# Kernel tuning notes

Measured on AMD Instinct MI355X. Metric: run time of the kernel, lower is better.

The kernel has to match this reference:

```python
import jax, jax.numpy as jnp
import numpy as np

N, E, IN_DIM, HID, TOWERS, NG = 20000, 320000, 16, 50, 5, 64
FO = HID // TOWERS  # out channels per tower = 10
EPS_BN = 1e-5
EPS_STD = 1e-5  # PyG StdAggregation: sqrt(relu(var) + 1e-5)


def setup_inputs() -> dict:
    key = jax.random.key(0)
    ks = jax.random.split(key, 24)
    rn = lambda k, shape: jax.random.normal(k, shape, dtype=jnp.float32) * 0.1
    F0, F1 = IN_DIM, HID
    return {
        "x": jax.random.normal(ks[0], (N, IN_DIM), dtype=jnp.float32),
        "edge_index": jax.random.randint(ks[1], (2, E), 0, N),
        "batch": jnp.sort(jax.random.randint(ks[2], (N,), 0, NG)),
        # conv0: pre Linear(2*F0 -> F0) per tower, post Linear(13*F0 -> FO) per tower, lin Linear(HID->HID)
        "pre_W0": rn(ks[3], (TOWERS, F0, 2 * F0)), "pre_b0": rn(ks[4], (TOWERS, F0)),
        "post_W0": rn(ks[5], (TOWERS, FO, 13 * F0)), "post_b0": rn(ks[6], (TOWERS, FO)),
        "lin_W0": rn(ks[7], (HID, HID)), "lin_b0": rn(ks[8], (HID,)),
        "gamma0": jnp.ones((HID,), jnp.float32), "beta0": jnp.zeros((HID,), jnp.float32),
        # conv1
        "pre_W1": rn(ks[9], (TOWERS, F1, 2 * F1)), "pre_b1": rn(ks[10], (TOWERS, F1)),
        "post_W1": rn(ks[11], (TOWERS, FO, 13 * F1)), "post_b1": rn(ks[12], (TOWERS, FO)),
        "lin_W1": rn(ks[13], (HID, HID)), "lin_b1": rn(ks[14], (HID,)),
        "gamma1": jnp.ones((HID,), jnp.float32), "beta1": jnp.zeros((HID,), jnp.float32),
        # head MLP: HID->50->25->1
        "mlp_W1": rn(ks[15], (50, HID)), "mlp_b1": rn(ks[16], (50,)),
        "mlp_W2": rn(ks[17], (25, 50)), "mlp_b2": rn(ks[18], (25,)),
        "mlp_W3": rn(ks[19], (1, 25)), "mlp_b3": rn(ks[20], (1,)),
    }


def pna_conv(x, src, dst, deg, avg_log, pre_W, pre_b, post_W, post_b, lin_W, lin_b):
    # x: [N, F]; divide_input=False -> every tower sees the full F features.
    n, Fi = x.shape
    T = pre_W.shape[0]
    # message: h = cat([x_i, x_j]) = cat([x[dst], x[src]]), then per-tower pre-MLP (1 Linear)
    h = jnp.concatenate([x[dst], x[src]], axis=-1)                  # [E, 2F]
    hs = jnp.einsum('ef,tgf->etg', h, pre_W) + pre_b                # [E, T, F]
    flat = hs.reshape(hs.shape[0], T * Fi)                          # [E, T*F]
    # multi-aggregation: mean / min / max / std, scattered to dst
    s = jax.ops.segment_sum(flat, dst, num_segments=n)
    s2 = jax.ops.segment_sum(flat * flat, dst, num_segments=n)
    mn = jax.ops.segment_min(flat, dst, num_segments=n)
    mx = jax.ops.segment_max(flat, dst, num_segments=n)
    degc = jnp.maximum(deg, 1.0)[:, None]
    mean = s / degc
    var = s2 / degc - mean * mean
    std = jnp.sqrt(jax.nn.relu(var) + EPS_STD)
    has = (deg > 0)[:, None]
    mn = jnp.where(has, mn, 0.0)
    mx = jnp.where(has, mx, 0.0)
    agg = jnp.concatenate([mean.reshape(n, T, Fi), mn.reshape(n, T, Fi),
                           mx.reshape(n, T, Fi), std.reshape(n, T, Fi)], axis=-1)  # [N,T,4F]
    # degree scalers: identity, amplification, attenuation
    amp = (jnp.log(jnp.maximum(deg, 1.0) + 1.0) / avg_log)[:, None, None]
    out = jnp.concatenate([jnp.broadcast_to(x[:, None, :], (n, T, Fi)),
                           agg, agg * amp, agg / amp], axis=-1)      # [N, T, 13F]
    out = jnp.einsum('ntf,tgf->ntg', out, post_W) + post_b          # [N, T, FO]
    return out.reshape(n, T * post_W.shape[1]) @ lin_W.T + lin_b    # [N, HID]


def _bn_relu(h, g, b):
    mu = h.mean(axis=0)
    v = jnp.mean((h - mu) ** 2, axis=0)  # biased var, torch BN training-mode normalization
    return jax.nn.relu(g * (h - mu) / jnp.sqrt(v + EPS_BN) + b)


def reference(x, edge_index, batch,
              pre_W0, pre_b0, post_W0, post_b0, lin_W0, lin_b0, gamma0, beta0,
              pre_W1, pre_b1, post_W1, post_b1, lin_W1, lin_b1, gamma1, beta1,
              mlp_W1, mlp_b1, mlp_W2, mlp_b2, mlp_W3, mlp_b3):
    src, dst = edge_index[0], edge_index[1]
    n = x.shape[0]
    deg = jax.ops.segment_sum(jnp.ones((src.shape[0],), jnp.float32), dst, num_segments=n)
    avg_log = jnp.mean(jnp.log(deg + 1.0))  # PNA avg_deg['log'] from this graph's degree histogram
    # NOTE: zip(convs, batch_norms) in the torch forward applies only num_conv_layer=2 convs.
    h = pna_conv(x, src, dst, deg, avg_log, pre_W0, pre_b0, post_W0, post_b0, lin_W0, lin_b0)
    h = _bn_relu(h, gamma0, beta0)
    h = pna_conv(h, src, dst, deg, avg_log, pre_W1, pre_b1, post_W1, post_b1, lin_W1, lin_b1)
    h = _bn_relu(h, gamma1, beta1)
    cnt = jax.ops.segment_sum(jnp.ones((n,), jnp.float32), batch, num_segments=NG)
    pooled = jax.ops.segment_sum(h, batch, num_segments=NG) / jnp.maximum(cnt, 1.0)[:, None]
    h = jax.nn.relu(pooled @ mlp_W1.T + mlp_b1)
    h = jax.nn.relu(h @ mlp_W2.T + mlp_b2)
    return h @ mlp_W3.T + mlp_b3  # [NG, 1]
```

## Files before the change

kernel.cpp:

```cpp
#include <hip/hip_runtime.h>
#include <math.h>
#include <float.h>

#define NN 20000
#define EE 320000
#define INDIM 16
#define HID 50
#define TW 5
#define FO 10
#define NGROUPS 64

typedef float f4 __attribute__((ext_vector_type(4)));
typedef float f2 __attribute__((ext_vector_type(2)));

__device__ inline f4 f4_min(f4 a, f4 b) {
    f4 r; r.x = fminf(a.x, b.x); r.y = fminf(a.y, b.y);
    r.z = fminf(a.z, b.z); r.w = fminf(a.w, b.w); return r;
}
__device__ inline f4 f4_max(f4 a, f4 b) {
    f4 r; r.x = fmaxf(a.x, b.x); r.y = fmaxf(a.y, b.y);
    r.z = fmaxf(a.z, b.z); r.w = fmaxf(a.w, b.w); return r;
}
__device__ inline float sh3sum(float v, int g0, int G_) {
    return v + __shfl(v, g0 + G_, 64) + __shfl(v, g0 + 2 * G_, 64);
}
__device__ inline float sh3min(float v, int g0, int G_) {
    return fminf(fminf(v, __shfl(v, g0 + G_, 64)), __shfl(v, g0 + 2 * G_, 64));
}
__device__ inline float sh3max(float v, int g0, int G_) {
    return fmaxf(fmaxf(v, __shfl(v, g0 + G_, 64)), __shfl(v, g0 + 2 * G_, 64));
}
__device__ inline void acc4(float& acc, f4 w, float a0, float a1, float a2, float a3) {
    acc += w.x * a0; acc += w.y * a1; acc += w.z * a2; acc += w.w * a3;
}

__global__ void k_deg(const int* __restrict__ dst, int* __restrict__ deg) {
    int e = blockIdx.x * 256 + threadIdx.x;
    if (e < EE) atomicAdd(&deg[dst[e]], 1);
}

__global__ void k_scan(const int* __restrict__ deg, int* __restrict__ offsets,
                       float* __restrict__ scal) {
    __shared__ int part[1024];
    __shared__ float fred[1024];
    const int CH = 20;
    int tid = threadIdx.x;
    int base = tid * CH;
    int loc[CH];
    int s = 0; float fs = 0.f;
    for (int c = 0; c < CH; ++c) {
        int idx = base + c;
        int v = (idx < NN) ? deg[idx] : 0;
        loc[c] = s; s += v;
        if (idx < NN) fs += logf((float)v + 1.0f);
    }
    part[tid] = s; fred[tid] = fs; __syncthreads();
    for (int off = 1; off < 1024; off <<= 1) {
        int v = (tid >= off) ? part[tid - off] : 0;
        __syncthreads();
        part[tid] += v;
        __syncthreads();
    }
    int pre = (tid > 0) ? part[tid - 1] : 0;
    for (int c = 0; c < CH; ++c) {
        int idx = base + c;
        if (idx < NN) offsets[idx] = pre + loc[c];
    }
    if (tid == 0) offsets[NN] = part[1023];
    for (int off = 512; off > 0; off >>= 1) {
        if (tid < off) fred[tid] += fred[tid + off];
        __syncthreads();
    }
    if (tid == 0) scal[0] = fred[0] / (float)NN;
}

__global__ void k_fill(const int* __restrict__ src, const int* __restrict__ dst,
                       const int* __restrict__ offsets, int* __restrict__ cursor,
                       int* __restrict__ csr_src) {
    int e = blockIdx.x * 256 + threadIdx.x;
    if (e < EE) {
        int d = dst[e];
        int pos = offsets[d] + atomicAdd(&cursor[d], 1);
        csr_src[pos] = src[e];
    }
}

__global__ void k_pack(const float* __restrict__ preW0, const float* __restrict__ preW1,
                       const float* __restrict__ postW0, const float* __restrict__ postW1,
                       const float* __restrict__ linW0, const float* __restrict__ linW1,
                       float* __restrict__ preWt0, float* __restrict__ preWt1,
                       float* __restrict__ Wx0, float* __restrict__ Wid0,
                       float* __restrict__ Wamp0, float* __restrict__ Watt0,
                       float* __restrict__ Wx1, float* __restrict__ Wid1,
                       float* __restrict__ Wamp1, float* __restrict__ Watt1,
                       float* __restrict__ Lt0, float* __restrict__ Lt1) {
    int idx = blockIdx.x * 256 + threadIdx.x;
    int job = blockIdx.y;
    int q = idx >> 8, k = (idx >> 2) & 63, j = idx & 3;
    switch (job) {
    case 0:
        if (idx < 32 * 80) { int c = idx / 80, r = idx % 80; preWt0[idx] = preW0[r * 32 + c]; }
        break;
    case 1:
        if (idx < 100 * 256) { int c = idx / 256, r = idx % 256; preWt1[idx] = (r < 250) ? preW1[r * 100 + c] : 0.f; }
        break;
    case 2:
        if (idx < 4 * 256) { int f = q * 4 + j; Wx0[idx] = (k < HID) ? postW0[k * 208 + f] : 0.f; }
        break;
    case 3:
        if (idx < 16 * 256) { int s = q / 4, f = (q % 4) * 4 + j; Wid0[idx] = (k < HID) ? postW0[k * 208 + (1 + s) * 16 + f] : 0.f; }
        break;
    case 4:
        if (idx < 16 * 256) { int s = q / 4, f = (q % 4) * 4 + j; Wamp0[idx] = (k < HID) ? postW0[k * 208 + (5 + s) * 16 + f] : 0.f; }
        break;
    case 5:
        if (idx < 16 * 256) { int s = q / 4, f = (q % 4) * 4 + j; Watt0[idx] = (k < HID) ? postW0[k * 208 + (9 + s) * 16 + f] : 0.f; }
        break;
    case 6:
        if (idx < 13 * 256) { int f = q * 4 + j; Wx1[idx] = (f < 50 && k < HID) ? postW1[k * 650 + f] : 0.f; }
        break;
    case 7:
        if (idx < 52 * 256) { int s = q / 13, f = (q % 13) * 4 + j; Wid1[idx] = (f < 50 && k < HID) ? postW1[k * 650 + (1 + s) * 50 + f] : 0.f; }
        break;
    case 8:
        if (idx < 52 * 256) { int s = q / 13, f = (q % 13) * 4 + j; Wamp1[idx] = (f < 50 && k < HID) ? postW1[k * 650 + (5 + s) * 50 + f] : 0.f; }
        break;
    case 9:
        if (idx < 52 * 256) { int s = q / 13, f = (q % 13) * 4 + j; Watt1[idx] = (f < 50 && k < HID) ? postW1[k * 650 + (9 + s) * 50 + f] : 0.f; }
        break;
    case 10:
        if (idx < 13 * 256) { int f = q * 4 + j; Lt0[idx] = (f < 50 && k < HID) ? linW0[k * 50 + f] : 0.f; }
        break;
    case 11:
        if (idx < 13 * 256) { int f = q * 4 + j; Lt1[idx] = (f < 50 && k < HID) ? linW1[k * 50 + f] : 0.f; }
        break;
    }
}

template <int F, int TF, int TFP, bool BN>
__global__ __launch_bounds__(256, 4) void k_gemm_CP(
    const float* __restrict__ x, const float* __restrict__ preWt,
    const float* __restrict__ b,
    const float* __restrict__ bnacc, const float* __restrict__ gam,
    const float* __restrict__ bet,
    float* __restrict__ C, float* __restrict__ P) {
    const int NODES = 16;
    __shared__ float xs[NODES * F];
    int tid = threadIdx.x;
    int base = blockIdx.x * NODES;
    for (int idx = tid; idx < NODES * F; idx += 256) {
        float v = x[(size_t)base * F + idx];
        if (BN) {
            int c = idx % F;
            float mu = bnacc[c] * (1.f / NN);
            float var = bnacc[64 + c] * (1.f / NN) - mu * mu;
            v = fmaxf(gam[c] * (v - mu) * rsqrtf(var + 1e-5f) + bet[c], 0.f);
        }
        xs[idx] = v;
    }
    __syncthreads();
    if (tid < TF) {
        float accC[NODES], accP[NODES];
#pragma unroll
        for (int n = 0; n < NODES; ++n) { accC[n] = 0.f; accP[n] = 0.f; }
        for (int f = 0; f < F; ++f) {
            float wl = preWt[f * TFP + tid];
            float wr = preWt[(F + f) * TFP + tid];
#pragma unroll
            for (int n = 0; n < NODES; ++n) {
                float xv = xs[n * F + f];
                accC[n] += xv * wl;
                accP[n] += xv * wr;
            }
        }
        float bb = b[tid];
        for (int n = 0; n < NODES; ++n) {
            C[((size_t)(base + n)) * TFP + tid] = accC[n] + bb;
            P[((size_t)(base + n)) * TFP + tid] = accP[n];
        }
    } else if (tid < TFP) {
        for (int n = 0; n < NODES; ++n) {
            C[((size_t)(base + n)) * TFP + tid] = 0.f;
            P[((size_t)(base + n)) * TFP + tid] = 0.f;
        }
    }
}

template <int F, int TFPG, int TFPL, int EP, int SQ, int SQX, bool AF4, bool BNIN>
__global__ __launch_bounds__(512, 6) void k_conv(
    const float* __restrict__ xin, const float* __restrict__ C, const float* __restrict__ P,
    const int* __restrict__ offsets, const int* __restrict__ csr,
    const float* __restrict__ scal,
    const float* __restrict__ Wx, const float* __restrict__ Wid,
    const float* __restrict__ Wamp, const float* __restrict__ Watt,
    const float* __restrict__ postb, const float* __restrict__ Lt,
    const float* __restrict__ linb,
    const float* __restrict__ bn_in, const float* __restrict__ g_in,
    const float* __restrict__ b_in,
    float* __restrict__ hout, float* __restrict__ bn_out) {
    const int GP = TFPG / 4;
    const int GL = TFPL / 4;
    __shared__ __align__(16) float sAgg[8][5][TFPL];
    __shared__ __align__(16) float sY[8][52];
    int t = threadIdx.x, w = t >> 6, lane = t & 63;
    int i = blockIdx.x * 8 + w;
    int beg = offsets[i], end = offsets[i + 1];
    int d = end - beg;

    {
        int g = (EP == 1) ? lane : (lane % GL);
        int e = (EP == 1) ? 0 : (lane / GL);
        bool act = (EP == 1) ? (lane < GL) : (e < EP);
        f4 S = {0.f, 0.f, 0.f, 0.f}, S2 = {0.f, 0.f, 0.f, 0.f};
        f4 MN = {FLT_MAX, FLT_MAX, FLT_MAX, FLT_MAX};
        f4 MX = {-FLT_MAX, -FLT_MAX, -FLT_MAX, -FLT_MAX};
        const f4* __restrict__ Pv = (const f4*)P;
        if (act) {
            if (EP == 1) {
                int j = beg;
                for (; j + 4 <= end; j += 4) {
                    int s0 = csr[j], s1 = csr[j + 1], s2 = csr[j + 2], s3 = csr[j + 3];
                    f4 a = Pv[(size_t)s0 * GP + g];
                    f4 b = Pv[(size_t)s1 * GP + g];
                    f4 c = Pv[(size_t)s2 * GP + g];
                    f4 dd = Pv[(size_t)s3 * GP + g];
                    S += a; S2 += a * a; MN = f4_min(MN, a); MX = f4_max(MX, a);
                    S += b; S2 += b * b; MN = f4_min(MN, b); MX = f4_max(MX, b);
                    S += c; S2 += c * c; MN = f4_min(MN, c); MX = f4_max(MX, c);
                    S += dd; S2 += dd * dd; MN = f4_min(MN, dd); MX = f4_max(MX, dd);
                }
                for (; j < end; ++j) {
                    int s0 = csr[j];
                    f4 a = Pv[(size_t)s0 * GP + g];
                    S += a; S2 += a * a; MN = f4_min(MN, a); MX = f4_max(MX, a);
                }
            } else {
                int j = beg + e;
                for (; j + EP < end; j += 2 * EP) {
                    int s0 = csr[j], s1 = csr[j + EP];
                    f4 a = Pv[(size_t)s0 * GP + g];
                    f4 b = Pv[(size_t)s1 * GP + g];
                    S += a; S2 += a * a; MN = f4_min(MN, a); MX = f4_max(MX, a);
                    S += b; S2 += b * b; MN = f4_min(MN, b); MX = f4_max(MX, b);
                }
                if (j < end) {
                    int s0 = csr[j];
                    f4 a = Pv[(size_t)s0 * GP + g];
                    S += a; S2 += a * a; MN = f4_min(MN, a); MX = f4_max(MX, a);
                }
            }
        }
        if (EP == 3) {
            int g0 = lane % GL;
            S.x = sh3sum(S.x, g0, GL); S.y = sh3sum(S.y, g0, GL);
            S.z = sh3sum(S.z, g0, GL); S.w = sh3sum(S.w, g0, GL);
            S2.x = sh3sum(S2.x, g0, GL); S2.y = sh3sum(S2.y, g0, GL);
            S2.z = sh3sum(S2.z, g0, GL); S2.w = sh3sum(S2.w, g0, GL);
            MN.x = sh3min(MN.x, g0, GL); MN.y = sh3min(MN.y, g0, GL);
            MN.z = sh3min(MN.z, g0, GL); MN.w = sh3min(MN.w, g0, GL);
            MX.x = sh3max(MX.x, g0, GL); MX.y = sh3max(MX.y, g0, GL);
            MX.z = sh3max(MX.z, g0, GL); MX.w = sh3max(MX.w, g0, GL);
        }
        if (lane < GL) {
            f4 Cv = ((const f4*)C)[(size_t)i * GP + lane];
            float degf = (float)d;
            float rdegc = 1.0f / fmaxf(degf, 1.0f);
            f4 mean, sq, var, stdv, mnv, mxv;
            mean.x = (degf * Cv.x + S.x) * rdegc; mean.y = (degf * Cv.y + S.y) * rdegc;
            mean.z = (degf * Cv.z + S.z) * rdegc; mean.w = (degf * Cv.w + S.w) * rdegc;
            sq.x = degf * Cv.x * Cv.x + 2.f * Cv.x * S.x + S2.x;
            sq.y = degf * Cv.y * Cv.y + 2.f * Cv.y * S.y + S2.y;
            sq.z = degf * Cv.z * Cv.z + 2.f * Cv.z * S.z + S2.z;
            sq.w = degf * Cv.w * Cv.w + 2.f * Cv.w * S.w + S2.w;
            var.x = sq.x * rdegc - mean.x * mean.x; var.y = sq.y * rdegc - mean.y * mean.y;
            var.z = sq.z * rdegc - mean.z * mean.z; var.w = sq.w * rdegc - mean.w * mean.w;
            stdv.x = sqrtf(fmaxf(var.x, 0.f) + 1e-5f); stdv.y = sqrtf(fmaxf(var.y, 0.f) + 1e-5f);
            stdv.z = sqrtf(fmaxf(var.z, 0.f) + 1e-5f); stdv.w = sqrtf(fmaxf(var.w, 0.f) + 1e-5f);
            if (d > 0) {
                mnv.x = Cv.x + MN.x; mnv.y = Cv.y + MN.y; mnv.z = Cv.z + MN.z; mnv.w = Cv.w + MN.w;
                mxv.x = Cv.x + MX.x; mxv.y = Cv.y + MX.y; mxv.z = Cv.z + MX.z; mxv.w = Cv.w + MX.w;
            } else {
                mnv = (f4){0.f, 0.f, 0.f, 0.f}; mxv = mnv;
            }
            ((f4*)&sAgg[w][0][0])[lane] = mean;
            ((f4*)&sAgg[w][1][0])[lane] = mnv;
            ((f4*)&sAgg[w][2][0])[lane] = mxv;
            ((f4*)&sAgg[w][3][0])[lane] = stdv;
        }
    }
    if (BNIN) {
        if (lane < F) {
            float hv = xin[(size_t)i * F + lane];
            float mu = bn_in[lane] * (1.f / NN);
            float var = bn_in[64 + lane] * (1.f / NN) - mu * mu;
            sAgg[w][4][lane] = fmaxf(g_in[lane] * (hv - mu) * rsqrtf(var + 1e-5f) + b_in[lane], 0.f);
        } else if (lane < SQX * 4) {
            sAgg[w][4][lane] = 0.f;
        }
    } else {
        if (lane < F) sAgg[w][4][lane] = xin[(size_t)i * F + lane];
        else if (lane < SQX * 4) sAgg[w][4][lane] = 0.f;
    }
    float amp = logf(fmaxf((float)d, 1.f) + 1.f) / scal[0];
    float ia = 1.0f / amp;
    __syncthreads();

    int kk = (lane < HID) ? lane : (HID - 1);
    int tw = kk / FO;
    const f4* __restrict__ Wxv = (const f4*)Wx;
    const f4* __restrict__ Wiv = (const f4*)Wid;
    const f4* __restrict__ Wav = (const f4*)Wamp;
    const f4* __restrict__ Wtv = (const f4*)Watt;
    float y0 = 0.f, y1 = 0.f, y2 = 0.f;
#pragma unroll
    for (int q = 0; q < SQX; ++q) {
        f4 wv = Wxv[q * 64 + lane];
        f4 a = *(const f4*)(&sAgg[w][4][4 * q]);
        acc4(y0, wv, a.x, a.y, a.z, a.w);
    }
#pragma unroll
    for (int s = 0; s < 4; ++s) {
        const float* __restrict__ A = &sAgg[w][s][tw * F];
#pragma unroll 4
        for (int q = 0; q < SQ; ++q) {
            f4 wi = Wiv[(s * SQ + q) * 64 + lane];
            f4 wa = Wav[(s * SQ + q) * 64 + lane];
            f4 wt = Wtv[(s * SQ + q) * 64 + lane];
            float a0, a1, a2, a3;
            if constexpr (AF4) {
                f4 av = *(const f4*)(A + 4 * q);
                a0 = av.x; a1 = av.y; a2 = av.z; a3 = av.w;
            } else {
                f2 u = *(const f2*)(A + 4 * q);
                f2 v = *(const f2*)(A + 4 * q + 2);
                a0 = u.x; a1 = u.y; a2 = v.x; a3 = v.y;
            }
            acc4(y0, wi, a0, a1, a2, a3);
            acc4(y1, wa, a0, a1, a2, a3);
            acc4(y2, wt, a0, a1, a2, a3);
        }
    }
    float y = postb[kk] + y0 + amp * y1 + ia * y2;
    if (lane < HID) sY[w][lane] = y;
    else if (lane < 52) sY[w][lane] = 0.f;

    const f4* __restrict__ Lv = (const f4*)Lt;
    float o = linb[kk];
#pragma unroll
    for (int q = 0; q < 13; ++q) {
        f4 lv = Lv[q * 64 + lane];
        f4 sv = *(const f4*)(&sY[w][4 * q]);
        acc4(o, lv, sv.x, sv.y, sv.z, sv.w);
    }
    if (lane < HID) hout[(size_t)i * HID + lane] = o;

    float ov = (lane < HID) ? o : 0.f;
    sAgg[w][0][lane] = ov;
    sAgg[w][1][lane] = ov * ov;
    __syncthreads();
    if (t < 64 && lane < HID) {
        float s = 0.f, s2 = 0.f;
#pragma unroll
        for (int w2 = 0; w2 < 8; ++w2) {
            s += sAgg[w2][0][lane];
            s2 += sAgg[w2][1][lane];
        }
        atomicAdd(&bn_out[lane], s);
        atomicAdd(&bn_out[64 + lane], s2);
    }
}

__global__ void k_head(const float* __restrict__ h, const int* __restrict__ batch,
                       const float* __restrict__ bnacc, const float* __restrict__ gam,
                       const float* __restrict__ bet,
                       const float* __restrict__ W1, const float* __restrict__ b1,
                       const float* __restrict__ W2, const float* __restrict__ b2,
                       const float* __restrict__ W3, const float* __restrict__ b3,
                       float* __restrict__ out) {
    __shared__ float sp[HID], h1[50], h2[25];
    __shared__ int sbound[2];
    int g = blockIdx.x, tid = threadIdx.x;
    if (tid < 2) {
        int target = g + tid;
        int lo = 0, hi = NN;
        while (lo < hi) {
            int mid = (lo + hi) >> 1;
            if (batch[mid] < target) lo = mid + 1; else hi = mid;
        }
        sbound[tid] = lo;
    }
    __syncthreads();
    int beg = sbound[0], end = sbound[1];
    if (tid < HID) {
        float mu = bnacc[tid] * (1.f / NN);
        float var = bnacc[64 + tid] * (1.f / NN) - mu * mu;
        float sc = gam[tid] * rsqrtf(var + 1e-5f);
        float sh = bet[tid] - mu * sc;
        float s0 = 0.f, s1 = 0.f, s2 = 0.f, s3 = 0.f;
        int n = beg;
        for (; n + 4 <= end; n += 4) {
            s0 += fmaxf(fmaf(h[(size_t)n * HID + tid], sc, sh), 0.f);
            s1 += fmaxf(fmaf(h[(size_t)(n + 1) * HID + tid], sc, sh), 0.f);
            s2 += fmaxf(fmaf(h[(size_t)(n + 2) * HID + tid], sc, sh), 0.f);
            s3 += fmaxf(fmaf(h[(size_t)(n + 3) * HID + tid], sc, sh), 0.f);
        }
        for (; n < end; ++n) s0 += fmaxf(fmaf(h[(size_t)n * HID + tid], sc, sh), 0.f);
        sp[tid] = (s0 + s1 + s2 + s3) / fmaxf((float)(end - beg), 1.0f);
    }
    __syncthreads();
    if (tid < 50) {
        float a = b1[tid];
        for (int k = 0; k < HID; ++k) a += W1[tid * HID + k] * sp[k];
        h1[tid] = fmaxf(a, 0.f);
    }
    __syncthreads();
    if (tid < 25) {
        float a = b2[tid];
        for (int k = 0; k < 50; ++k) a += W2[tid * 50 + k] * h1[k];
        h2[tid] = fmaxf(a, 0.f);
    }
    __syncthreads();
    if (tid == 0) {
        float a = b3[0];
        for (int k = 0; k < 25; ++k) a += W3[k] * h2[k];
        out[g] = a;
    }
}

extern "C" void kernel_launch(void* const* d_in, const int* in_sizes, int n_in,
                              void* d_out, int out_size, void* d_ws, size_t ws_size,
                              hipStream_t stream) {
    const float* x      = (const float*)d_in[0];
    const int*   ei     = (const int*)d_in[1];
    const int*   batch  = (const int*)d_in[2];
    const float* preW0  = (const float*)d_in[3];
    const float* preb0  = (const float*)d_in[4];
    const float* postW0 = (const float*)d_in[5];
    const float* postb0 = (const float*)d_in[6];
    const float* linW0  = (const float*)d_in[7];
    const float* linb0  = (const float*)d_in[8];
    const float* gamma0 = (const float*)d_in[9];
    const float* beta0  = (const float*)d_in[10];
    const float* preW1  = (const float*)d_in[11];
    const float* preb1  = (const float*)d_in[12];
    const float* postW1 = (const float*)d_in[13];
    const float* postb1 = (const float*)d_in[14];
    const float* linW1  = (const float*)d_in[15];
    const float* linb1  = (const float*)d_in[16];
    const float* gamma1 = (const float*)d_in[17];
    const float* beta1  = (const float*)d_in[18];
    const float* mW1    = (const float*)d_in[19];
    const float* mb1    = (const float*)d_in[20];
    const float* mW2    = (const float*)d_in[21];
    const float* mb2    = (const float*)d_in[22];
    const float* mW3    = (const float*)d_in[23];
    const float* mb3    = (const float*)d_in[24];
    float* out = (float*)d_out;
    (void)in_sizes; (void)n_in; (void)out_size; (void)ws_size;

    char* ws = (char*)d_ws;
    size_t off = 0;
    auto alloc = [&](size_t bytes) -> void* {
        void* p = ws + off;
        off += (bytes + 255) & ~(size_t)255;
        return p;
    };
    int*   deg     = (int*)alloc((size_t)NN * 4);
    int*   cursor  = (int*)alloc((size_t)NN * 4);
    float* bnacc0  = (float*)alloc(128 * 4);
    float* bnacc1  = (float*)alloc(128 * 4);
    size_t zero_bytes = off;
    int*   offsets = (int*)alloc((size_t)(NN + 1) * 4);
    int*   csr_src = (int*)alloc((size_t)EE * 4);
    float* scal    = (float*)alloc(64);
    float* preWt0  = (float*)alloc((size_t)32 * 80 * 4);
    float* preWt1  = (float*)alloc((size_t)100 * 256 * 4);
    float* Wx0     = (float*)alloc((size_t)4 * 256 * 4);
    float* Wid0    = (float*)alloc((size_t)16 * 256 * 4);
    float* Wamp0   = (float*)alloc((size_t)16 * 256 * 4);
    float* Watt0   = (float*)alloc((size_t)16 * 256 * 4);
    float* Wx1     = (float*)alloc((size_t)13 * 256 * 4);
    float* Wid1    = (float*)alloc((size_t)52 * 256 * 4);
    float* Wamp1   = (float*)alloc((size_t)52 * 256 * 4);
    float* Watt1   = (float*)alloc((size_t)52 * 256 * 4);
    float* Lt0     = (float*)alloc((size_t)13 * 256 * 4);
    float* Lt1     = (float*)alloc((size_t)13 * 256 * 4);
    float* Cbuf    = (float*)alloc((size_t)NN * 256 * 4);
    float* Pbuf    = (float*)alloc((size_t)NN * 256 * 4);
    float* h1buf   = (float*)alloc((size_t)NN * HID * 4);
    float* h2buf   = (float*)alloc((size_t)NN * HID * 4);

    const int* src = ei;
    const int* dst = ei + EE;

    hipMemsetAsync(ws, 0, zero_bytes, stream);

    k_pack<<<dim3(100, 12), 256, 0, stream>>>(preW0, preW1, postW0, postW1, linW0, linW1,
                                              preWt0, preWt1, Wx0, Wid0, Wamp0, Watt0,
                                              Wx1, Wid1, Wamp1, Watt1, Lt0, Lt1);
    k_deg<<<EE / 256, 256, 0, stream>>>(dst, deg);
    k_scan<<<1, 1024, 0, stream>>>(deg, offsets, scal);
    k_fill<<<EE / 256, 256, 0, stream>>>(src, dst, offsets, cursor, csr_src);

    k_gemm_CP<INDIM, 80, 80, false><<<NN / 16, 256, 0, stream>>>(
        x, preWt0, preb0, nullptr, nullptr, nullptr, Cbuf, Pbuf);
    k_conv<INDIM, 80, 80, 3, 4, 4, true, false><<<NN / 8, 512, 0, stream>>>(
        x, Cbuf, Pbuf, offsets, csr_src, scal, Wx0, Wid0, Wamp0, Watt0, postb0, Lt0, linb0,
        nullptr, nullptr, nullptr, h1buf, bnacc0);

    k_gemm_CP<HID, 250, 256, true><<<NN / 16, 256, 0, stream>>>(
        h1buf, preWt1, preb1, bnacc0, gamma0, beta0, Cbuf, Pbuf);
    k_conv<HID, 256, 252, 1, 13, 13, false, true><<<NN / 8, 512, 0, stream>>>(
        h1buf, Cbuf, Pbuf, offsets, csr_src, scal, Wx1, Wid1, Wamp1, Watt1, postb1, Lt1, linb1,
        bnacc0, gamma0, beta0, h2buf, bnacc1);

    k_head<<<NGROUPS, 64, 0, stream>>>(h2buf, batch, bnacc1, gamma1, beta1,
                                       mW1, mb1, mW2, mb2, mW3, mb3, out);
}
```

Baseline: 344.7 us.

## Process two nodes per wavefront in k_conv to reuse post-MLP weight loads

Each wavefront now handles two destination nodes, gathering aggregates for both in sequence and then running the post-tower and linear matvecs for both at once. Each weight vector is loaded from global memory once and applied to two nodes, halving weight traffic per node. Blocks shrink to 256 threads (4 waves, 8 nodes) and the launch bounds change to match. The cost is more registers per thread and a serialized gather phase within each wave, which may reduce latency hiding in the neighbor gather.

```diff
diff --git a/kernel.cpp b/kernel.cpp
--- a/kernel.cpp
+++ b/kernel.cpp
@@ -187,7 +187,7 @@
 }
 
 template <int F, int TFPG, int TFPL, int EP, int SQ, int SQX, bool AF4, bool BNIN>
-__global__ __launch_bounds__(512, 6) void k_conv(
+__global__ __launch_bounds__(256, 4) void k_conv(
     const float* __restrict__ xin, const float* __restrict__ C, const float* __restrict__ P,
     const int* __restrict__ offsets, const int* __restrict__ csr,
     const float* __restrict__ scal,
@@ -200,14 +200,19 @@
     float* __restrict__ hout, float* __restrict__ bn_out) {
     const int GP = TFPG / 4;
     const int GL = TFPL / 4;
-    __shared__ __align__(16) float sAgg[8][5][TFPL];
+    __shared__ __align__(16) float sAgg[8][4][TFPL];
+    __shared__ __align__(16) float sX[8][64];
     __shared__ __align__(16) float sY[8][52];
+    __shared__ float sBN[4][2][64];
     int t = threadIdx.x, w = t >> 6, lane = t & 63;
-    int i = blockIdx.x * 8 + w;
-    int beg = offsets[i], end = offsets[i + 1];
-    int d = end - beg;
-
-    {
+    int ibase = blockIdx.x * 8 + 2 * w;
+    float ampv[2], iav[2];
+
+    for (int nn = 0; nn < 2; ++nn) {
+        int nd = 2 * w + nn;
+        int i = ibase + nn;
+        int beg = offsets[i], end = offsets[i + 1];
+        int d = end - beg;
         int g = (EP == 1) ? lane : (lane % GL);
         int e = (EP == 1) ? 0 : (lane / GL);
         bool act = (EP == 1) ? (lane < GL) : (e < EP);
@@ -282,89 +287,107 @@
             } else {
                 mnv = (f4){0.f, 0.f, 0.f, 0.f}; mxv = mnv;
             }
-            ((f4*)&sAgg[w][0][0])[lane] = mean;
-            ((f4*)&sAgg[w][1][0])[lane] = mnv;
-            ((f4*)&sAgg[w][2][0])[lane] = mxv;
-            ((f4*)&sAgg[w][3][0])[lane] = stdv;
-        }
-    }
-    if (BNIN) {
-        if (lane < F) {
-            float hv = xin[(size_t)i * F + lane];
-            float mu = bn_in[lane] * (1.f / NN);
-            float var = bn_in[64 + lane] * (1.f / NN) - mu * mu;
-            sAgg[w][4][lane] = fmaxf(g_in[lane] * (hv - mu) * rsqrtf(var + 1e-5f) + b_in[lane], 0.f);
-        } else if (lane < SQX * 4) {
-            sAgg[w][4][lane] = 0.f;
-        }
-    } else {
-        if (lane < F) sAgg[w][4][lane] = xin[(size_t)i * F + lane];
-        else if (lane < SQX * 4) sAgg[w][4][lane] = 0.f;
-    }
-    float amp = logf(fmaxf((float)d, 1.f) + 1.f) / scal[0];
-    float ia = 1.0f / amp;
-    __syncthreads();
-
+            ((f4*)&sAgg[nd][0][0])[lane] = mean;
+            ((f4*)&sAgg[nd][1][0])[lane] = mnv;
+            ((f4*)&sAgg[nd][2][0])[lane] = mxv;
+            ((f4*)&sAgg[nd][3][0])[lane] = stdv;
+        }
+        if (BNIN) {
+            if (lane < F) {
+                float hv = xin[(size_t)i * F + lane];
+                float mu = bn_in[lane] * (1.f / NN);
+                float var = bn_in[64 + lane] * (1.f / NN) - mu * mu;
+                sX[nd][lane] = fmaxf(g_in[lane] * (hv - mu) * rsqrtf(var + 1e-5f) + b_in[lane], 0.f);
+            } else if (lane < SQX * 4) {
+                sX[nd][lane] = 0.f;
+            }
+        } else {
+            if (lane < F) sX[nd][lane] = xin[(size_t)i * F + lane];
+            else if (lane < SQX * 4) sX[nd][lane] = 0.f;
+        }
+        float amp = logf(fmaxf((float)d, 1.f) + 1.f) / scal[0];
+        ampv[nn] = amp; iav[nn] = 1.0f / amp;
+    }
+    __syncthreads();
+
+    int nd0 = 2 * w, nd1 = 2 * w + 1;
+    int i0 = ibase, i1 = ibase + 1;
     int kk = (lane < HID) ? lane : (HID - 1);
     int tw = kk / FO;
     const f4* __restrict__ Wxv = (const f4*)Wx;
     const f4* __restrict__ Wiv = (const f4*)Wid;
     const f4* __restrict__ Wav = (const f4*)Wamp;
     const f4* __restrict__ Wtv = (const f4*)Watt;
-    float y0 = 0.f, y1 = 0.f, y2 = 0.f;
+    float y0a = 0.f, y1a = 0.f, y2a = 0.f, y0b = 0.f, y1b = 0.f, y2b = 0.f;
 #pragma unroll
     for (int q = 0; q < SQX; ++q) {
         f4 wv = Wxv[q * 64 + lane];
-        f4 a = *(const f4*)(&sAgg[w][4][4 * q]);
-        acc4(y0, wv, a.x, a.y, a.z, a.w);
+        f4 a0 = *(const f4*)(&sX[nd0][4 * q]);
+        f4 a1 = *(const f4*)(&sX[nd1][4 * q]);
+        acc4(y0a, wv, a0.x, a0.y, a0.z, a0.w);
+        acc4(y0b, wv, a1.x, a1.y, a1.z, a1.w);
     }
 #pragma unroll
     for (int s = 0; s < 4; ++s) {
-        const float* __restrict__ A = &sAgg[w][s][tw * F];
+        const float* __restrict__ A0 = &sAgg[nd0][s][tw * F];
+        const float* __restrict__ A1 = &sAgg[nd1][s][tw * F];
 #pragma unroll 4
         for (int q = 0; q < SQ; ++q) {
             f4 wi = Wiv[(s * SQ + q) * 64 + lane];
             f4 wa = Wav[(s * SQ + q) * 64 + lane];
             f4 wt = Wtv[(s * SQ + q) * 64 + lane];
-            float a0, a1, a2, a3;
+            float a00, a01, a02, a03, a10, a11, a12, a13;
             if constexpr (AF4) {
-                f4 av = *(const f4*)(A + 4 * q);
-                a0 = av.x; a1 = av.y; a2 = av.z; a3 = av.w;
+                f4 v0 = *(const f4*)(A0 + 4 * q);
+                f4 v1 = *(const f4*)(A1 + 4 * q);
+                a00 = v0.x; a01 = v0.y; a02 = v0.z; a03 = v0.w;
+                a10 = v1.x; a11 = v1.y; a12 = v1.z; a13 = v1.w;
             } else {
-                f2 u = *(const f2*)(A + 4 * q);
-                f2 v = *(const f2*)(A + 4 * q + 2);
-                a0 = u.x; a1 = u.y; a2 = v.x; a3 = v.y;
+                f2 p0 = *(const f2*)(A0 + 4 * q);
+                f2 p1 = *(const f2*)(A0 + 4 * q + 2);
+                f2 q0 = *(const f2*)(A1 + 4 * q);
+                f2 q1 = *(const f2*)(A1 + 4 * q + 2);
+                a00 = p0.x; a01 = p0.y; a02 = p1.x; a03 = p1.y;
+                a10 = q0.x; a11 = q0.y; a12 = q1.x; a13 = q1.y;
             }
-            acc4(y0, wi, a0, a1, a2, a3);
-            acc4(y1, wa, a0, a1, a2, a3);
-            acc4(y2, wt, a0, a1, a2, a3);
-        }
-    }
-    float y = postb[kk] + y0 + amp * y1 + ia * y2;
-    if (lane < HID) sY[w][lane] = y;
-    else if (lane < 52) sY[w][lane] = 0.f;
+            acc4(y0a, wi, a00, a01, a02, a03);
+            acc4(y1a, wa, a00, a01, a02, a03);
+            acc4(y2a, wt, a00, a01, a02, a03);
+            acc4(y0b, wi, a10, a11, a12, a13);
+            acc4(y1b, wa, a10, a11, a12, a13);
+            acc4(y2b, wt, a10, a11, a12, a13);
+        }
+    }
+    float pb = postb[kk];
+    float ya = pb + y0a + ampv[0] * y1a + iav[0] * y2a;
+    float yb = pb + y0b + ampv[1] * y1b + iav[1] * y2b;
+    if (lane < HID) { sY[nd0][lane] = ya; sY[nd1][lane] = yb; }
+    else if (lane < 52) { sY[nd0][lane] = 0.f; sY[nd1][lane] = 0.f; }
 
     const f4* __restrict__ Lv = (const f4*)Lt;
-    float o = linb[kk];
+    float lb = linb[kk];
+    float oa = lb, ob = lb;
 #pragma unroll
     for (int q = 0; q < 13; ++q) {
         f4 lv = Lv[q * 64 + lane];
-        f4 sv = *(const f4*)(&sY[w][4 * q]);
-        acc4(o, lv, sv.x, sv.y, sv.z, sv.w);
-    }
-    if (lane < HID) hout[(size_t)i * HID + lane] = o;
-
-    float ov = (lane < HID) ? o : 0.f;
-    sAgg[w][0][lane] = ov;
-    sAgg[w][1][lane] = ov * ov;
+        f4 s0 = *(const f4*)(&sY[nd0][4 * q]);
+        f4 s1 = *(const f4*)(&sY[nd1][4 * q]);
+        acc4(oa, lv, s0.x, s0.y, s0.z, s0.w);
+        acc4(ob, lv, s1.x, s1.y, s1.z, s1.w);
+    }
+    if (lane < HID) {
+        hout[(size_t)i0 * HID + lane] = oa;
+        hout[(size_t)i1 * HID + lane] = ob;
+    }
+
+    float sv = 0.f, sv2 = 0.f;
+    if (lane < HID) { sv = oa + ob; sv2 = oa * oa + ob * ob; }
+    sBN[w][0][lane] = sv;
+    sBN[w][1][lane] = sv2;
     __syncthreads();
     if (t < 64 && lane < HID) {
-        float s = 0.f, s2 = 0.f;
-#pragma unroll
-        for (int w2 = 0; w2 < 8; ++w2) {
-            s += sAgg[w2][0][lane];
-            s2 += sAgg[w2][1][lane];
-        }
+        float s = sBN[0][0][lane] + sBN[1][0][lane] + sBN[2][0][lane] + sBN[3][0][lane];
+        float s2 = sBN[0][1][lane] + sBN[1][1][lane] + sBN[2][1][lane] + sBN[3][1][lane];
         atomicAdd(&bn_out[lane], s);
         atomicAdd(&bn_out[64 + lane], s2);
     }
@@ -504,13 +527,13 @@
 
     k_gemm_CP<INDIM, 80, 80, false><<<NN / 16, 256, 0, stream>>>(
         x, preWt0, preb0, nullptr, nullptr, nullptr, Cbuf, Pbuf);
-    k_conv<INDIM, 80, 80, 3, 4, 4, true, false><<<NN / 8, 512, 0, stream>>>(
+    k_conv<INDIM, 80, 80, 3, 4, 4, true, false><<<NN / 8, 256, 0, stream>>>(
         x, Cbuf, Pbuf, offsets, csr_src, scal, Wx0, Wid0, Wamp0, Watt0, postb0, Lt0, linb0,
         nullptr, nullptr, nullptr, h1buf, bnacc0);
 
     k_gemm_CP<HID, 250, 256, true><<<NN / 16, 256, 0, stream>>>(
         h1buf, preWt1, preb1, bnacc0, gamma0, beta0, Cbuf, Pbuf);
-    k_conv<HID, 256, 252, 1, 13, 13, false, true><<<NN / 8, 512, 0, stream>>>(
+    k_conv<HID, 256, 252, 1, 13, 13, false, true><<<NN / 8, 256, 0, stream>>>(
         h1buf, Cbuf, Pbuf, offsets, csr_src, scal, Wx1, Wid1, Wamp1, Watt1, postb1, Lt1, linb1,
         bnacc0, gamma0, beta0, h2buf, bnacc1);
 
```

New measurement: 325.2 us. 1.06x faster.
